# Kernel optimization log

Measured on AMD Instinct MI355X. Metric: run time of the kernel, lower is better.

The kernel has to match this reference:

```python
import jax, jax.numpy as jnp
import numpy as np
from jax import lax

T, B, V, H = 64, 1024, 128, 512
IMG_FEAT = 16 * 15 * 15


def _conv(x, w, b, pad):
    # x: [N,C,H,W], w: [O,I,kh,kw]
    y = lax.conv_general_dilated(x, w, (1, 1), [(pad, pad), (pad, pad)],
                                 dimension_numbers=('NCHW', 'OIHW', 'NCHW'))
    return y + b[None, :, None, None]


def _pool(x):
    return lax.reduce_window(x, -jnp.inf, lax.max, (1, 1, 2, 2), (1, 1, 2, 2), 'VALID')


def setup_inputs() -> dict:
    key = jax.random.key(0)
    ks = jax.random.split(key, 16)
    std = 1.0 / np.sqrt(H)
    u = lambda k, shape: jax.random.uniform(k, shape, jnp.float32, -std, std)
    return {
        'inp': jax.random.normal(ks[0], (T, B, V), jnp.float32),
        'img': jax.random.normal(ks[1], (B, 1, 64, 64), jnp.float32),
        'conv1_w': u(ks[2], (8, 1, 3, 3)),
        'conv1_b': u(ks[3], (8,)),
        'conv2_w': u(ks[4], (16, 8, 5, 5)),
        'conv2_b': u(ks[5], (16,)),
        'imgfc_w': u(ks[6], (IMG_FEAT, H)),
        'imgfc_b': u(ks[7], (H,)),
        'xh_w': u(ks[8], (V, 4 * H)),
        'xh_b': u(ks[9], (4 * H,)),
        'hh_w': u(ks[10], (H, 4 * H)),
        'hh_b': u(ks[11], (4 * H,)),
        'out_w': u(ks[12], (H, V)),
        'out_b': u(ks[13], (V,)),
    }


def reference(inp, img, conv1_w, conv1_b, conv2_w, conv2_b, imgfc_w, imgfc_b,
              xh_w, xh_b, hh_w, hh_b, out_w, out_b):
    t_len, batch, _ = inp.shape
    hid = hh_w.shape[0]

    # CNN image embedding: [B,1,64,64] -> [B,16,15,15] -> [B,H]
    e = jax.nn.relu(_conv(img, conv1_w, conv1_b, 1))
    e = _pool(e)
    e = jax.nn.relu(_conv(e, conv2_w, conv2_b, 1))
    e = _pool(e)
    e = e.reshape(batch, -1)
    e = jax.nn.relu(e @ imgfc_w + imgfc_b)
    img4 = jnp.concatenate([e, e, e, e], axis=1)  # [B, 4H], added at t==0

    # Precompute input-to-gate projections for all timesteps (batched GEMM)
    xg = jnp.einsum('tbv,vh->tbh', inp, xh_w) + xh_b  # [T, B, 4H]
    xg = xg.at[0].add(img4)

    def step(carry, xg_t):
        h, c = carry
        gates = xg_t + h @ hh_w + hh_b
        i, f, g, o = jnp.split(gates, 4, axis=1)  # chunk(4, dim=1) order: i,f,g,o
        i = jax.nn.sigmoid(i)
        f = jax.nn.sigmoid(f)
        o = jax.nn.sigmoid(o)
        g = jnp.tanh(g)
        c = f * c + i * g
        h = o * jnp.tanh(c)
        return (h, c), h

    h0 = jnp.zeros((batch, hid), inp.dtype)
    _, hs = lax.scan(step, (h0, h0), xg)  # hs: [T, B, H]

    logits = jnp.einsum('tbh,hv->tbv', hs, out_w) + out_b
    return jax.nn.log_softmax(logits, axis=-1)
```

## Files before the change

kernel.cpp:

```cpp
#include <hip/hip_runtime.h>

#define T_ 64
#define B_ 1024
#define V_ 128
#define H_ 512
#define KFC 3616

typedef short bf16x8 __attribute__((ext_vector_type(8)));
typedef short bf16x4 __attribute__((ext_vector_type(4)));
typedef float f32x4 __attribute__((ext_vector_type(4)));
typedef float f32x16 __attribute__((ext_vector_type(16)));
typedef int int4v __attribute__((ext_vector_type(4)));

#define ZERO16 ((f32x16){0.f,0.f,0.f,0.f,0.f,0.f,0.f,0.f,0.f,0.f,0.f,0.f,0.f,0.f,0.f,0.f})

__device__ __forceinline__ unsigned short f2bf(float f) {
    union { float f; unsigned int i; } v; v.f = f;
    unsigned int x = v.i;
    return (unsigned short)((x + 0x7FFFu + ((x >> 16) & 1u)) >> 16);
}
__device__ __forceinline__ float sigm(float x) { return 1.f / (1.f + __expf(-x)); }
__device__ __forceinline__ float tanh_fast(float x) {
    float ax = fabsf(x);
    float t = 1.f - 2.f / (__expf(2.f * ax) + 1.f);
    return copysignf(t, x);
}

__global__ __launch_bounds__(256) void cbias_k(const float* __restrict__ xh_b,
                                               const float* __restrict__ hh_b,
                                               float* __restrict__ cbias,
                                               unsigned int* __restrict__ ctr) {
    int i = blockIdx.x * 256 + threadIdx.x;
    cbias[i] = xh_b[i] + hh_b[i];
    if (i < 512) ctr[i] = 0u;
}

__global__ __launch_bounds__(256) void convx_k(const float* __restrict__ x,
                                               unsigned short* __restrict__ xbf) {
    int e = blockIdx.x * 256 + threadIdx.x;
    int t = e >> 13, r = e & 8191;
    int panel = r >> 10, b = r & 1023;
    const float* ip = x + ((size_t)t * 1024 + b) * 128 + panel * 16;
    unsigned short* op = xbf + (size_t)t * 131072 + panel * 16384 + b * 16;
#pragma unroll
    for (int h = 0; h < 2; ++h) {
        float4 f0 = *(const float4*)(ip + h * 8);
        float4 f1 = *(const float4*)(ip + h * 8 + 4);
        bf16x8 o;
        o[0] = (short)f2bf(f0.x); o[1] = (short)f2bf(f0.y);
        o[2] = (short)f2bf(f0.z); o[3] = (short)f2bf(f0.w);
        o[4] = (short)f2bf(f1.x); o[5] = (short)f2bf(f1.y);
        o[6] = (short)f2bf(f1.z); o[7] = (short)f2bf(f1.w);
        *(bf16x8*)(op + h * 8) = o;
    }
}

__global__ __launch_bounds__(256) void convw_k(const float* __restrict__ xw,
                                               const float* __restrict__ hw,
                                               unsigned short* __restrict__ wt) {
    int i = blockIdx.x * 256 + threadIdx.x;
    int n = i / 640, k = i - n * 640;
    float v = (k < 128) ? xw[k * 2048 + n] : hw[(k - 128) * 2048 + n];
    wt[i] = f2bf(v);
}

__global__ __launch_bounds__(256) void convow_k(const float* __restrict__ ow,
                                                unsigned short* __restrict__ wo) {
    int i = blockIdx.x * 256 + threadIdx.x;
    int n = i >> 9, k = i & 511;
    wo[i] = f2bf(ow[k * 128 + n]);
}

__global__ __launch_bounds__(256) void convfw_k(const float* __restrict__ w,
                                                unsigned short* __restrict__ wn) {
    __shared__ float ts[16][257];
    int bx = blockIdx.x;
    int k0 = (bx >> 1) * 16, n0 = (bx & 1) * 256;
    int tid = threadIdx.x;
#pragma unroll
    for (int r = 0; r < 16; ++r)
        ts[r][tid] = w[(size_t)(k0 + r) * 512 + n0 + tid];
    __syncthreads();
    unsigned short* op = wn + (size_t)(n0 + tid) * KFC + k0;
    bf16x8 o0, o1;
#pragma unroll
    for (int r = 0; r < 8; ++r) o0[r] = (short)f2bf(ts[r][tid]);
#pragma unroll
    for (int r = 0; r < 8; ++r) o1[r] = (short)f2bf(ts[8 + r][tid]);
    *(bf16x8*)op = o0;
    *(bf16x8*)(op + 8) = o1;
    if (k0 == 3584) {
        bf16x8 z = (bf16x8){0,0,0,0,0,0,0,0};
        *(bf16x8*)(op + 16) = z;
        *(bf16x8*)(op + 24) = z;
    }
}

__global__ __launch_bounds__(256) void conv1_k(const float* __restrict__ img,
                                               const float* __restrict__ w,
                                               const float* __restrict__ bias,
                                               float* __restrict__ out) {
    int id = blockIdx.x * 256 + threadIdx.x;
    int px = id & 31, py = (id >> 5) & 31, b = id >> 10;
    const float* ip = img + b * 4096;
    float in4[4][4];
#pragma unroll
    for (int dy = 0; dy < 4; ++dy) {
        int iy = 2 * py + dy - 1;
#pragma unroll
        for (int dx = 0; dx < 4; ++dx) {
            int ix = 2 * px + dx - 1;
            in4[dy][dx] = (iy >= 0 && iy < 64 && ix >= 0 && ix < 64) ? ip[iy * 64 + ix] : 0.f;
        }
    }
    float* op = out + b * 8192 + py * 32 + px;
#pragma unroll
    for (int oc = 0; oc < 8; ++oc) {
        float wv[9];
#pragma unroll
        for (int t = 0; t < 9; ++t) wv[t] = w[oc * 9 + t];
        float bs = bias[oc];
        float m = -3.4e38f;
#pragma unroll
        for (int sy = 0; sy < 2; ++sy)
#pragma unroll
        for (int sx = 0; sx < 2; ++sx) {
            float acc = bs;
#pragma unroll
            for (int ky = 0; ky < 3; ++ky)
#pragma unroll
            for (int kx = 0; kx < 3; ++kx)
                acc += in4[sy + ky][sx + kx] * wv[ky * 3 + kx];
            m = fmaxf(m, acc);
        }
        op[oc * 1024] = fmaxf(m, 0.f);
    }
}

__device__ __forceinline__ int c2idx(int ic, int y, int x) {
    return ((ic * 34 + y) * 2 + (x & 1)) * 18 + (x >> 1);
}
__global__ __launch_bounds__(256) void conv2_k(const float* __restrict__ in,
                                               const float* __restrict__ w,
                                               const float* __restrict__ bias,
                                               unsigned short* __restrict__ feat) {
    __shared__ float in_s[8 * 34 * 36];
    __shared__ float w_s[3200];
    __shared__ float b_s[16];
    int tid = threadIdx.x, b = blockIdx.x;
    for (int e = tid; e < 8 * 34 * 34; e += 256) {
        int ic = e / 1156, r = e - ic * 1156;
        int y = r / 34, xx = r - y * 34;
        float v = 0.f;
        if (y >= 1 && y <= 32 && xx >= 1 && xx <= 32)
            v = in[b * 8192 + ic * 1024 + (y - 1) * 32 + (xx - 1)];
        in_s[c2idx(ic, y, xx)] = v;
    }
    for (int e = tid; e < 3200; e += 256) w_s[e] = w[e];
    if (tid < 16) b_s[tid] = bias[tid];
    if (tid < 16) feat[(size_t)b * KFC + 3600 + tid] = 0;
    __syncthreads();
    for (int o = tid; o < 3600; o += 256) {
        int oc = o / 225, p = o - oc * 225;
        int py = p / 15, px = p - py * 15;
        int y0 = 2 * py;
        float a00, a01, a10, a11;
        a00 = a01 = a10 = a11 = b_s[oc];
        for (int ic = 0; ic < 8; ++ic) {
            const float* wp = w_s + (oc * 8 + ic) * 25;
            float cur[6], nxt[6];
#pragma unroll
            for (int xx = 0; xx < 6; ++xx) cur[xx] = in_s[c2idx(ic, y0, 2 * px + xx)];
#pragma unroll
            for (int ky = 0; ky < 5; ++ky) {
#pragma unroll
                for (int xx = 0; xx < 6; ++xx) nxt[xx] = in_s[c2idx(ic, y0 + ky + 1, 2 * px + xx)];
#pragma unroll
                for (int kx = 0; kx < 5; ++kx) {
                    float wv = wp[ky * 5 + kx];
                    a00 += cur[kx    ] * wv;
                    a01 += cur[kx + 1] * wv;
                    a10 += nxt[kx    ] * wv;
                    a11 += nxt[kx + 1] * wv;
                }
#pragma unroll
                for (int xx = 0; xx < 6; ++xx) cur[xx] = nxt[xx];
            }
        }
        float mx = fmaxf(fmaxf(a00, a01), fmaxf(a10, a11));
        feat[(size_t)b * KFC + o] = f2bf(fmaxf(mx, 0.f));
    }
}

#define MFMA16(a, b, c) __builtin_amdgcn_mfma_f32_16x16x32_bf16((a), (b), (c), 0, 0, 0)
#define MFMA32(a, b, c) __builtin_amdgcn_mfma_f32_32x32x16_bf16((a), (b), (c), 0, 0, 0)

__global__ __launch_bounds__(256) void imgfc_mfma(const unsigned short* __restrict__ A,
                                                  const unsigned short* __restrict__ Wn,
                                                  const float* __restrict__ bias,
                                                  float* __restrict__ E) {
    const int tid = threadIdx.x;
    const int wv = tid >> 6, lane = tid & 63;
    const int quad = lane >> 4, l16 = lane & 15;
    const int row0 = blockIdx.x * 64 + wv * 16;
    const int col0 = blockIdx.y * 64;
    const unsigned short* ap = A + (size_t)(row0 + l16) * KFC + quad * 8;
    f32x4 acc[4];
#pragma unroll
    for (int tn = 0; tn < 4; ++tn) acc[tn] = (f32x4){0.f, 0.f, 0.f, 0.f};
    for (int k0 = 0; k0 < KFC; k0 += 32) {
        bf16x8 a = *(const bf16x8*)(ap + k0);
#pragma unroll
        for (int tn = 0; tn < 4; ++tn) {
            bf16x8 b = *(const bf16x8*)(Wn + (size_t)(col0 + tn * 16 + l16) * KFC + k0 + quad * 8);
            acc[tn] = MFMA16(a, b, acc[tn]);
        }
    }
#pragma unroll
    for (int reg = 0; reg < 4; ++reg) {
        int r = row0 + quad * 4 + reg;
#pragma unroll
        for (int tn = 0; tn < 4; ++tn) {
            int cI = col0 + tn * 16 + l16;
            E[(size_t)r * 512 + cI] = fmaxf(acc[tn][reg] + bias[cI], 0.f);
        }
    }
}

__global__ __launch_bounds__(512, 2) void lstm_persist(
        const unsigned short* __restrict__ xbf,
        const unsigned short* __restrict__ wt,
        const float* __restrict__ cbias,
        const float* __restrict__ eimg,
        unsigned short* __restrict__ hs,
        unsigned int* __restrict__ ctr) {
    extern __shared__ unsigned char smem[];
    unsigned short* w_s = (unsigned short*)smem;
    float* xbuf = (float*)(smem + 82944);
    unsigned short* scr = (unsigned short*)(smem + 82944 + 32768);
    const int tid = threadIdx.x;
    const int wave = tid >> 6, lane = tid & 63;
    const int l31 = lane & 31, lh = lane >> 5, h8 = lh * 8;
    const int rt = wave & 3, ks = wave >> 2;
    const int rg = blockIdx.x & 7;
    const int jblk = blockIdx.x >> 3;
    const int j0 = jblk * 16;
    const int rowbase = rg * 128 + rt * 32;
    unsigned int* flags = ctr + rg * 64;

    for (int e = tid; e < 64 * 80; e += 512) {
        int r = e / 80, c8 = (e - r * 80) * 8;
        int g = r >> 4, rr = r & 15;
        *(bf16x8*)(w_s + r * 648 + c8) =
            *(const bf16x8*)(wt + (size_t)(g * 512 + j0 + rr) * 640 + c8);
    }
    f32x4 cbi[2], cbf_[2], cbg[2], cbo[2];
#pragma unroll
    for (int qq = 0; qq < 2; ++qq) {
        cbi[qq]  = *(const f32x4*)(cbias +        j0 + qq * 8 + lh * 4);
        cbf_[qq] = *(const f32x4*)(cbias +  512 + j0 + qq * 8 + lh * 4);
        cbg[qq]  = *(const f32x4*)(cbias + 1024 + j0 + qq * 8 + lh * 4);
        cbo[qq]  = *(const f32x4*)(cbias + 1536 + j0 + qq * 8 + lh * 4);
    }
    __syncthreads();

    float cst[8];
    f32x16 acc0 = ZERO16, acc1 = ZERO16;

    {
        const unsigned short* xp = xbf + (size_t)(ks * 4) * 16384
                                       + (size_t)(rowbase + l31) * 16 + h8;
        bf16x8 xreg[4];
#pragma unroll
        for (int kk = 0; kk < 4; ++kk) xreg[kk] = *(const bf16x8*)(xp + kk * 16384);
        __builtin_amdgcn_sched_barrier(0);
        const unsigned short* wx = w_s + (size_t)l31 * 648 + ks * 64 + h8;
#pragma unroll
        for (int kk = 0; kk < 4; ++kk) {
            bf16x8 a0 = *(const bf16x8*)(wx + kk * 16);
            bf16x8 a1 = *(const bf16x8*)(wx + 32 * 648 + kk * 16);
            acc0 = MFMA32(a0, xreg[kk], acc0);
            acc1 = MFMA32(a1, xreg[kk], acc1);
        }
    }

#pragma unroll 1
    for (int t = 0; t < T_; ++t) {
        if (t > 0) {
            asm volatile("s_waitcnt vmcnt(0)" ::: "memory");
            __syncthreads();
            if (tid == 0)
                __hip_atomic_store(flags + jblk, (unsigned int)t,
                                   __ATOMIC_RELAXED, __HIP_MEMORY_SCOPE_AGENT);
            if (wave == 0) {
                int guard = 0;
                for (;;) {
                    unsigned int v = __hip_atomic_load(flags + l31,
                                                       __ATOMIC_RELAXED, __HIP_MEMORY_SCOPE_AGENT);
                    if (__all((int)(v >= (unsigned int)t)) || ++guard > (1 << 20)) break;
                }
            }
            __syncthreads();
            const unsigned short* hp = hs + (size_t)(t - 1) * (B_ * H_)
                                          + (size_t)(ks * 16) * 16384
                                          + (size_t)(rowbase + l31) * 16 + h8;
            bf16x8 breg[16];
#pragma unroll
            for (int kk = 0; kk < 16; ++kk) breg[kk] = *(const bf16x8*)(hp + (size_t)kk * 16384);
            __builtin_amdgcn_sched_barrier(0);
            const unsigned short* wh = w_s + (size_t)l31 * 648 + 128 + ks * 256 + h8;
#pragma unroll
            for (int kk = 0; kk < 16; ++kk) {
                bf16x8 a0 = *(const bf16x8*)(wh + kk * 16);
                bf16x8 a1 = *(const bf16x8*)(wh + 32 * 648 + kk * 16);
                acc0 = MFMA32(a0, breg[kk], acc0);
                acc1 = MFMA32(a1, breg[kk], acc1);
            }
        }
        if (ks == 1) {
            float* xb = xbuf + rt * 2048 + lane * 4;
#pragma unroll
            for (int q = 0; q < 4; ++q)
                *(f32x4*)(xb + q * 256) =
                    (f32x4){acc0[q*4], acc0[q*4+1], acc0[q*4+2], acc0[q*4+3]};
#pragma unroll
            for (int q = 0; q < 4; ++q)
                *(f32x4*)(xb + (4 + q) * 256) =
                    (f32x4){acc1[q*4], acc1[q*4+1], acc1[q*4+2], acc1[q*4+3]};
        }
        __syncthreads();
        if (ks == 0) {
            const float* xb = xbuf + rt * 2048 + lane * 4;
#pragma unroll
            for (int q = 0; q < 4; ++q) {
                f32x4 p = *(const f32x4*)(xb + q * 256);
                acc0[q*4] += p[0]; acc0[q*4+1] += p[1]; acc0[q*4+2] += p[2]; acc0[q*4+3] += p[3];
            }
#pragma unroll
            for (int q = 0; q < 4; ++q) {
                f32x4 p = *(const f32x4*)(xb + (4 + q) * 256);
                acc1[q*4] += p[0]; acc1[q*4+1] += p[1]; acc1[q*4+2] += p[2]; acc1[q*4+3] += p[3];
            }
            unsigned short* sw = scr + rt * 512 + l31 * 16;
#pragma unroll
            for (int qq = 0; qq < 2; ++qq) {
                f32x4 ea4 = (f32x4){0.f, 0.f, 0.f, 0.f};
                if (t == 0)
                    ea4 = *(const f32x4*)(eimg + (size_t)(rowbase + l31) * 512
                                               + j0 + qq * 8 + lh * 4);
                bf16x4 hv;
#pragma unroll
                for (int jj = 0; jj < 4; ++jj) {
                    int ci = qq * 4 + jj;
                    float iv = sigm(acc0[ci]     + cbi[qq][jj]  + ea4[jj]);
                    float fv = sigm(acc0[8 + ci] + cbf_[qq][jj] + ea4[jj]);
                    float gv = tanh_fast(acc1[ci] + cbg[qq][jj] + ea4[jj]);
                    float ov = sigm(acc1[8 + ci] + cbo[qq][jj] + ea4[jj]);
                    float co = (t == 0) ? 0.f : cst[ci];
                    float cn = fv * co + iv * gv;
                    cst[ci] = cn;
                    hv[jj] = (short)f2bf(ov * tanh_fast(cn));
                }
                *(bf16x4*)(sw + qq * 8 + lh * 4) = hv;
            }
            asm volatile("s_waitcnt lgkmcnt(0)" ::: "memory");
            int4v v = *(const int4v*)(scr + rt * 512 + lane * 8);
            unsigned short* gp = hs + (size_t)t * (B_ * H_) + (size_t)jblk * 16384
                                    + (size_t)(rowbase + (lane >> 1)) * 16 + (lane & 1) * 8;
            asm volatile("global_store_dwordx4 %0, %1, off sc0 sc1" :: "v"(gp), "v"(v) : "memory");
        }
        if (t < T_ - 1) {
            acc0 = ZERO16; acc1 = ZERO16;
            const unsigned short* xp = xbf + (size_t)(t + 1) * 131072
                                           + (size_t)(ks * 4) * 16384
                                           + (size_t)(rowbase + l31) * 16 + h8;
            bf16x8 xreg[4];
#pragma unroll
            for (int kk = 0; kk < 4; ++kk) xreg[kk] = *(const bf16x8*)(xp + kk * 16384);
            __builtin_amdgcn_sched_barrier(0);
            const unsigned short* wx = w_s + (size_t)l31 * 648 + ks * 64 + h8;
#pragma unroll
            for (int kk = 0; kk < 4; ++kk) {
                bf16x8 a0 = *(const bf16x8*)(wx + kk * 16);
                bf16x8 a1 = *(const bf16x8*)(wx + 32 * 648 + kk * 16);
                acc0 = MFMA32(a0, xreg[kk], acc0);
                acc1 = MFMA32(a1, xreg[kk], acc1);
            }
        }
    }
}

__global__ __launch_bounds__(256, 2) void logits_mfma(
        const unsigned short* __restrict__ hs,
        const unsigned short* __restrict__ wo,
        const float* __restrict__ ob,
        float* __restrict__ out) {
    __shared__ unsigned short wos[128 * 264];
    const int tid = threadIdx.x;
    const int wave = tid >> 6, lane = tid & 63;
    const int quad = lane >> 4, l16 = lane & 15;
    const int row0 = blockIdx.x * 64 + wave * 16;
    const int trow = row0 >> 10;
    const int b0 = row0 & 1023;
    const unsigned short* hbase = hs + (size_t)trow * (B_ * H_)
                                     + (size_t)(b0 + l16) * 16 + (quad & 1) * 8;
    f32x4 acc[8];
#pragma unroll
    for (int q = 0; q < 8; ++q) acc[q] = (f32x4){0.f, 0.f, 0.f, 0.f};

    for (int half = 0; half < 2; ++half) {
        __syncthreads();
        for (int e = tid; e < 128 * 32; e += 256) {
            int n = e >> 5, c8 = (e & 31) * 8;
            *(bf16x8*)(wos + n * 264 + c8) = *(const bf16x8*)(wo + n * 512 + half * 256 + c8);
        }
        __syncthreads();
#pragma unroll
        for (int ki = 0; ki < 8; ++ki) {
            int p = half * 16 + ki * 2 + (quad >> 1);
            bf16x8 a = *(const bf16x8*)(hbase + (size_t)p * 16384);
#pragma unroll
            for (int tn = 0; tn < 8; ++tn) {
                bf16x8 b = *(const bf16x8*)(wos + (tn * 16 + l16) * 264 + ki * 32 + quad * 8);
                acc[tn] = MFMA16(a, b, acc[tn]);
            }
        }
    }
    float bia[8];
#pragma unroll
    for (int tn = 0; tn < 8; ++tn) bia[tn] = ob[tn * 16 + l16];
#pragma unroll
    for (int reg = 0; reg < 4; ++reg) {
        float v[8];
        float m = -3.4e38f;
#pragma unroll
        for (int tn = 0; tn < 8; ++tn) { v[tn] = acc[tn][reg] + bia[tn]; m = fmaxf(m, v[tn]); }
#pragma unroll
        for (int off = 1; off < 16; off <<= 1) m = fmaxf(m, __shfl_xor(m, off, 64));
        float s = 0.f;
#pragma unroll
        for (int tn = 0; tn < 8; ++tn) s += __expf(v[tn] - m);
#pragma unroll
        for (int off = 1; off < 16; off <<= 1) s += __shfl_xor(s, off, 64);
        float z = m + __logf(s);
        int row = row0 + quad * 4 + reg;
        float* op = out + (size_t)row * 128;
#pragma unroll
        for (int tn = 0; tn < 8; ++tn) op[tn * 16 + l16] = v[tn] - z;
    }
}

extern "C" void kernel_launch(void* const* d_in, const int* in_sizes, int n_in,
                              void* d_out, int out_size, void* d_ws, size_t ws_size,
                              hipStream_t stream) {
    const float* inp     = (const float*)d_in[0];
    const float* img     = (const float*)d_in[1];
    const float* conv1_w = (const float*)d_in[2];
    const float* conv1_b = (const float*)d_in[3];
    const float* conv2_w = (const float*)d_in[4];
    const float* conv2_b = (const float*)d_in[5];
    const float* imgfc_w = (const float*)d_in[6];
    const float* imgfc_b = (const float*)d_in[7];
    const float* xh_w    = (const float*)d_in[8];
    const float* xh_b    = (const float*)d_in[9];
    const float* hh_w    = (const float*)d_in[10];
    const float* hh_b    = (const float*)d_in[11];
    const float* out_w   = (const float*)d_in[12];
    const float* out_b   = (const float*)d_in[13];

    char* ws = (char*)d_ws;
    unsigned short* hs  = (unsigned short*)(ws);
    float* conv1out     = (float*)(ws);
    unsigned short* feat= (unsigned short*)(ws + (32u << 20));
    unsigned short* wfc = (unsigned short*)(ws + (48u << 20));
    float* e            = (float*)(ws + (64u << 20));
    float* cbias        = (float*)(ws + (66u << 20));
    unsigned short* xbf = (unsigned short*)(ws + (67u << 20));
    unsigned short* wt  = (unsigned short*)(ws + (83u << 20));
    unsigned short* wo  = (unsigned short*)(ws + (86u << 20));
    unsigned int*  ctr  = (unsigned int*)(ws + (87u << 20));
    float* outp         = (float*)d_out;

    cbias_k<<<8, 256, 0, stream>>>(xh_b, hh_b, cbias, ctr);
    convx_k<<<(T_ * B_ * 8) / 256, 256, 0, stream>>>(inp, xbf);
    convw_k<<<(2048 * 640) / 256, 256, 0, stream>>>(xh_w, hh_w, wt);
    convow_k<<<(128 * 512) / 256, 256, 0, stream>>>(out_w, wo);
    convfw_k<<<450, 256, 0, stream>>>(imgfc_w, wfc);
    conv1_k<<<(B_ * 32 * 32) / 256, 256, 0, stream>>>(img, conv1_w, conv1_b, conv1out);
    conv2_k<<<B_, 256, 0, stream>>>(conv1out, conv2_w, conv2_b, feat);
    imgfc_mfma<<<dim3(16, 8), 256, 0, stream>>>(feat, wfc, imgfc_b, e);

    lstm_persist<<<256, 512, 82944 + 32768 + 4096, stream>>>(
        xbf, wt, cbias, e, hs, ctr);

    logits_mfma<<<(T_ * B_) / 64, 256, 0, stream>>>(hs, wo, out_b, outp);
}
```

Measured before the change: 838.8 us.

## Fuse weight-prep kernels and retile image FC operands into K-blocked layout

Merges the three small weight/bias conversion kernels into a single launch to cut launch overhead. It also changes the conv2 feature output and the transposed imgfc weight into a K-blocked layout of 32-element slabs. In this layout each MFMA K step reads contiguous 64-byte rows per slab instead of rows strided by the full 3616 length. The image FC kernel now computes 32 columns per block over a 16x16 grid, giving more blocks with fewer accumulators each. The padding rows of the last K block are zeroed in both operands to keep the tail correct.

```diff
diff --git a/kernel.cpp b/kernel.cpp
--- a/kernel.cpp
+++ b/kernel.cpp
@@ -26,13 +26,30 @@
     return copysignf(t, x);
 }
 
-__global__ __launch_bounds__(256) void cbias_k(const float* __restrict__ xh_b,
-                                               const float* __restrict__ hh_b,
-                                               float* __restrict__ cbias,
-                                               unsigned int* __restrict__ ctr) {
-    int i = blockIdx.x * 256 + threadIdx.x;
-    cbias[i] = xh_b[i] + hh_b[i];
-    if (i < 512) ctr[i] = 0u;
+__global__ __launch_bounds__(256) void prep_k(const float* __restrict__ xw,
+                                              const float* __restrict__ hw,
+                                              unsigned short* __restrict__ wt,
+                                              const float* __restrict__ ow,
+                                              unsigned short* __restrict__ wo,
+                                              const float* __restrict__ xh_b,
+                                              const float* __restrict__ hh_b,
+                                              float* __restrict__ cbias,
+                                              unsigned int* __restrict__ ctr) {
+    int bx = blockIdx.x, tid = threadIdx.x;
+    if (bx < 5120) {
+        int i = bx * 256 + tid;
+        int n = i / 640, k = i - n * 640;
+        float v = (k < 128) ? xw[k * 2048 + n] : hw[(k - 128) * 2048 + n];
+        wt[i] = f2bf(v);
+    } else if (bx < 5376) {
+        int i = (bx - 5120) * 256 + tid;
+        int n = i >> 9, k = i & 511;
+        wo[i] = f2bf(ow[k * 128 + n]);
+    } else {
+        int i = (bx - 5376) * 256 + tid;
+        cbias[i] = xh_b[i] + hh_b[i];
+        if (i < 512) ctr[i] = 0u;
+    }
 }
 
 __global__ __launch_bounds__(256) void convx_k(const float* __restrict__ x,
@@ -55,44 +72,25 @@
     }
 }
 
-__global__ __launch_bounds__(256) void convw_k(const float* __restrict__ xw,
-                                               const float* __restrict__ hw,
-                                               unsigned short* __restrict__ wt) {
-    int i = blockIdx.x * 256 + threadIdx.x;
-    int n = i / 640, k = i - n * 640;
-    float v = (k < 128) ? xw[k * 2048 + n] : hw[(k - 128) * 2048 + n];
-    wt[i] = f2bf(v);
-}
-
-__global__ __launch_bounds__(256) void convow_k(const float* __restrict__ ow,
-                                                unsigned short* __restrict__ wo) {
-    int i = blockIdx.x * 256 + threadIdx.x;
-    int n = i >> 9, k = i & 511;
-    wo[i] = f2bf(ow[k * 128 + n]);
-}
-
 __global__ __launch_bounds__(256) void convfw_k(const float* __restrict__ w,
                                                 unsigned short* __restrict__ wn) {
-    __shared__ float ts[16][257];
+    __shared__ float ts[32][257];
     int bx = blockIdx.x;
-    int k0 = (bx >> 1) * 16, n0 = (bx & 1) * 256;
+    int kb = bx >> 1, n0 = (bx & 1) * 256;
     int tid = threadIdx.x;
 #pragma unroll
-    for (int r = 0; r < 16; ++r)
-        ts[r][tid] = w[(size_t)(k0 + r) * 512 + n0 + tid];
+    for (int r = 0; r < 32; ++r) {
+        int k = kb * 32 + r;
+        ts[r][tid] = (k < 3600) ? w[(size_t)k * 512 + n0 + tid] : 0.f;
+    }
     __syncthreads();
-    unsigned short* op = wn + (size_t)(n0 + tid) * KFC + k0;
-    bf16x8 o0, o1;
-#pragma unroll
-    for (int r = 0; r < 8; ++r) o0[r] = (short)f2bf(ts[r][tid]);
-#pragma unroll
-    for (int r = 0; r < 8; ++r) o1[r] = (short)f2bf(ts[8 + r][tid]);
-    *(bf16x8*)op = o0;
-    *(bf16x8*)(op + 8) = o1;
-    if (k0 == 3584) {
-        bf16x8 z = (bf16x8){0,0,0,0,0,0,0,0};
-        *(bf16x8*)(op + 16) = z;
-        *(bf16x8*)(op + 24) = z;
+    unsigned short* op = wn + (size_t)kb * 16384 + (size_t)(n0 + tid) * 32;
+#pragma unroll
+    for (int m = 0; m < 4; ++m) {
+        bf16x8 o;
+#pragma unroll
+        for (int e = 0; e < 8; ++e) o[e] = (short)f2bf(ts[m * 8 + e][tid]);
+        *(bf16x8*)(op + m * 8) = o;
     }
 }
 
@@ -158,7 +156,7 @@
     }
     for (int e = tid; e < 3200; e += 256) w_s[e] = w[e];
     if (tid < 16) b_s[tid] = bias[tid];
-    if (tid < 16) feat[(size_t)b * KFC + 3600 + tid] = 0;
+    if (tid < 16) feat[(size_t)112 * 32768 + (size_t)b * 32 + 16 + tid] = 0;
     __syncthreads();
     for (int o = tid; o < 3600; o += 256) {
         int oc = o / 225, p = o - oc * 225;
@@ -188,42 +186,41 @@
             }
         }
         float mx = fmaxf(fmaxf(a00, a01), fmaxf(a10, a11));
-        feat[(size_t)b * KFC + o] = f2bf(fmaxf(mx, 0.f));
+        feat[(size_t)(o >> 5) * 32768 + (size_t)b * 32 + (o & 31)] = f2bf(fmaxf(mx, 0.f));
     }
 }
 
 #define MFMA16(a, b, c) __builtin_amdgcn_mfma_f32_16x16x32_bf16((a), (b), (c), 0, 0, 0)
 #define MFMA32(a, b, c) __builtin_amdgcn_mfma_f32_32x32x16_bf16((a), (b), (c), 0, 0, 0)
 
-__global__ __launch_bounds__(256) void imgfc_mfma(const unsigned short* __restrict__ A,
-                                                  const unsigned short* __restrict__ Wn,
+__global__ __launch_bounds__(256) void imgfc_mfma(const unsigned short* __restrict__ A2,
+                                                  const unsigned short* __restrict__ W2,
                                                   const float* __restrict__ bias,
                                                   float* __restrict__ E) {
     const int tid = threadIdx.x;
     const int wv = tid >> 6, lane = tid & 63;
     const int quad = lane >> 4, l16 = lane & 15;
     const int row0 = blockIdx.x * 64 + wv * 16;
-    const int col0 = blockIdx.y * 64;
-    const unsigned short* ap = A + (size_t)(row0 + l16) * KFC + quad * 8;
-    f32x4 acc[4];
-#pragma unroll
-    for (int tn = 0; tn < 4; ++tn) acc[tn] = (f32x4){0.f, 0.f, 0.f, 0.f};
-    for (int k0 = 0; k0 < KFC; k0 += 32) {
-        bf16x8 a = *(const bf16x8*)(ap + k0);
-#pragma unroll
-        for (int tn = 0; tn < 4; ++tn) {
-            bf16x8 b = *(const bf16x8*)(Wn + (size_t)(col0 + tn * 16 + l16) * KFC + k0 + quad * 8);
-            acc[tn] = MFMA16(a, b, acc[tn]);
-        }
+    const int col0 = blockIdx.y * 32;
+    const unsigned short* ap = A2 + (size_t)(row0 + l16) * 32 + quad * 8;
+    const unsigned short* bp0 = W2 + (size_t)(col0 + l16) * 32 + quad * 8;
+    const unsigned short* bp1 = W2 + (size_t)(col0 + 16 + l16) * 32 + quad * 8;
+    f32x4 acc0 = (f32x4){0.f, 0.f, 0.f, 0.f};
+    f32x4 acc1 = (f32x4){0.f, 0.f, 0.f, 0.f};
+#pragma unroll 4
+    for (int kb = 0; kb < 113; ++kb) {
+        bf16x8 a  = *(const bf16x8*)(ap  + (size_t)kb * 32768);
+        bf16x8 b0 = *(const bf16x8*)(bp0 + (size_t)kb * 16384);
+        bf16x8 b1 = *(const bf16x8*)(bp1 + (size_t)kb * 16384);
+        acc0 = MFMA16(a, b0, acc0);
+        acc1 = MFMA16(a, b1, acc1);
     }
 #pragma unroll
     for (int reg = 0; reg < 4; ++reg) {
         int r = row0 + quad * 4 + reg;
-#pragma unroll
-        for (int tn = 0; tn < 4; ++tn) {
-            int cI = col0 + tn * 16 + l16;
-            E[(size_t)r * 512 + cI] = fmaxf(acc[tn][reg] + bias[cI], 0.f);
-        }
+        int c0 = col0 + l16, c1 = col0 + 16 + l16;
+        E[(size_t)r * 512 + c0] = fmaxf(acc0[reg] + bias[c0], 0.f);
+        E[(size_t)r * 512 + c1] = fmaxf(acc1[reg] + bias[c1], 0.f);
     }
 }
 
@@ -481,14 +478,12 @@
     unsigned int*  ctr  = (unsigned int*)(ws + (87u << 20));
     float* outp         = (float*)d_out;
 
-    cbias_k<<<8, 256, 0, stream>>>(xh_b, hh_b, cbias, ctr);
+    prep_k<<<5384, 256, 0, stream>>>(xh_w, hh_w, wt, out_w, wo, xh_b, hh_b, cbias, ctr);
     convx_k<<<(T_ * B_ * 8) / 256, 256, 0, stream>>>(inp, xbf);
-    convw_k<<<(2048 * 640) / 256, 256, 0, stream>>>(xh_w, hh_w, wt);
-    convow_k<<<(128 * 512) / 256, 256, 0, stream>>>(out_w, wo);
-    convfw_k<<<450, 256, 0, stream>>>(imgfc_w, wfc);
+    convfw_k<<<226, 256, 0, stream>>>(imgfc_w, wfc);
     conv1_k<<<(B_ * 32 * 32) / 256, 256, 0, stream>>>(img, conv1_w, conv1_b, conv1out);
     conv2_k<<<B_, 256, 0, stream>>>(conv1out, conv2_w, conv2_b, feat);
-    imgfc_mfma<<<dim3(16, 8), 256, 0, stream>>>(feat, wfc, imgfc_b, e);
+    imgfc_mfma<<<dim3(16, 16), 256, 0, stream>>>(feat, wfc, imgfc_b, e);
 
     lstm_persist<<<256, 512, 82944 + 32768 + 4096, stream>>>(
         xbf, wt, cbias, e, hs, ctr);
```

New measurement: 740.1 us. 11.8% less time.
